# Optimization experiments

Hardware: AMD Instinct MI355X
Metric: run time of the kernel (lower is better)

## Reference

```python
import jax, jax.numpy as jnp
import numpy as np

N = 10000      # nodes
E = 80000      # directed edges (before self loops)
F_IN = 128     # input feature dim
OUT = 16       # out_channels (classes)


def setup_inputs() -> dict:
    key = jax.random.key(0)
    ks = jax.random.split(key, 20)
    p = lambda k, shape: (jax.random.normal(k, shape, jnp.float32) * 0.1)
    x = jax.random.normal(ks[0], (N, F_IN), jnp.float32)
    edge_index = jax.random.randint(ks[1], (2, E), 0, N, dtype=jnp.int64)
    return {
        "x": x, "edge_index": edge_index,
        # conv1: in=128 -> heads=10, ch=256
        "W1": p(ks[2], (F_IN, 10 * 256)), "as1": p(ks[3], (10, 256)), "ad1": p(ks[4], (10, 256)), "b1": jnp.zeros((10 * 256,), jnp.float32),
        # conv2: in=2560 -> heads=8, ch=56
        "W2": p(ks[5], (2560, 8 * 56)), "as2": p(ks[6], (8, 56)), "ad2": p(ks[7], (8, 56)), "b2": jnp.zeros((8 * 56,), jnp.float32),
        # conv3: in=448 -> heads=4, ch=32
        "W3": p(ks[8], (448, 4 * 32)), "as3": p(ks[9], (4, 32)), "ad3": p(ks[10], (4, 32)), "b3": jnp.zeros((4 * 32,), jnp.float32),
        # conv4: in=128 -> heads=1, ch=OUT, concat=False (mean over heads)
        "W4": p(ks[11], (128, 1 * OUT)), "as4": p(ks[12], (1, OUT)), "ad4": p(ks[13], (1, OUT)), "b4": jnp.zeros((OUT,), jnp.float32),
    }


def _gat_layer(x, src, dst, W, a_src, a_dst, b, heads, ch, concat, n):
    # linear projection -> [n, H, C]
    h = (x @ W).reshape(n, heads, ch)
    # per-node attention halves (PyG decomposition of a^T [h_i || h_j])
    e_src = jnp.einsum('nhc,hc->nh', h, a_src)
    e_dst = jnp.einsum('nhc,hc->nh', h, a_dst)
    # per-edge logits, LeakyReLU(0.2) as in PyG GATConv
    e = jax.nn.leaky_relu(e_src[src] + e_dst[dst], 0.2)  # [E', H]
    # segment softmax over edges grouped by destination node
    m = jax.ops.segment_max(e, dst, num_segments=n)
    m = jnp.where(jnp.isfinite(m), m, 0.0)
    ex = jnp.exp(e - m[dst])
    denom = jax.ops.segment_sum(ex, dst, num_segments=n)
    alpha = ex / (denom[dst] + 1e-16)  # [E', H]
    # weighted scatter-sum of source messages
    out = jax.ops.segment_sum(alpha[:, :, None] * h[src], dst, num_segments=n)  # [n, H, C]
    out = out.reshape(n, heads * ch) if concat else out.mean(axis=1)
    return out + b


def reference(x, edge_index, W1, as1, ad1, b1, W2, as2, ad2, b2,
              W3, as3, ad3, b3, W4, as4, ad4, b4):
    n = x.shape[0]
    loops = jnp.arange(n, dtype=edge_index.dtype)
    src = jnp.concatenate([edge_index[0], loops])  # add_self_loops=True
    dst = jnp.concatenate([edge_index[1], loops])
    lrelu = lambda t: jax.nn.leaky_relu(t, 0.1)  # outer activations in forward()
    h = lrelu(_gat_layer(x, src, dst, W1, as1, ad1, b1, 10, 256, True, n))
    h = lrelu(_gat_layer(h, src, dst, W2, as2, ad2, b2, 8, 56, True, n))
    h = lrelu(_gat_layer(h, src, dst, W3, as3, ad3, b3, 4, 32, True, n))
    h = lrelu(_gat_layer(h, src, dst, W4, as4, ad4, b4, 1, OUT, False, n))
    return jax.nn.softmax(h, axis=1)
```

## Files before the change

kernel.cpp:

```cpp
#include <hip/hip_runtime.h>
#include <math.h>

#define NNODES 10000
#define MPAD   10112
#define NEDGES 80000
#define ETOT   (NEDGES + NNODES)

typedef __attribute__((ext_vector_type(4))) float f32x4;
typedef __attribute__((ext_vector_type(8))) short bf16x8;
typedef __attribute__((ext_vector_type(4))) unsigned short u16x4;
typedef __attribute__((ext_vector_type(4))) unsigned int u32x4;

__device__ inline unsigned short f2bf(float f) {
    unsigned int u = __float_as_uint(f);
    unsigned int r = (u + 0x7fffu + ((u >> 16) & 1u)) >> 16;
    return (unsigned short)r;
}
__device__ inline float bf2f(unsigned short h) {
    return __uint_as_float(((unsigned int)h) << 16);
}
__device__ inline float lrelu01(float v) { return (v > 0.f) ? v : 0.1f * v; }
__device__ inline float lrelu02(float v) { return (v > 0.f) ? v : 0.2f * v; }

__global__ void count_deg(const int* __restrict__ ei, int* __restrict__ indeg,
                          int E, int n) {
    int i = blockIdx.x * blockDim.x + threadIdx.x;
    if (i >= E + n) return;
    int dst = (i < E) ? ei[E + i] : (i - E);
    atomicAdd(&indeg[dst], 1);
}

__global__ void scan_rowptr(const int* __restrict__ indeg, int* __restrict__ row_ptr,
                            int* __restrict__ cursor, int n) {
    __shared__ int sums[1024];
    int tid = threadIdx.x;
    int per = (n + 1023) / 1024;
    int start = tid * per;
    int end = start + per; if (end > n) end = n;
    int s = 0;
    for (int i = start; i < end; ++i) s += indeg[i];
    sums[tid] = s;
    __syncthreads();
    for (int off = 1; off < 1024; off <<= 1) {
        int v = (tid >= off) ? sums[tid - off] : 0;
        __syncthreads();
        sums[tid] += v;
        __syncthreads();
    }
    int excl = (tid == 0) ? 0 : sums[tid - 1];
    for (int i = start; i < end; ++i) {
        row_ptr[i] = excl;
        cursor[i]  = excl;
        excl += indeg[i];
    }
    if (tid == 1023) row_ptr[n] = sums[1023];
}

__global__ void scatter_edges(const int* __restrict__ ei, int* __restrict__ cursor,
                              int* __restrict__ col, int E, int n) {
    int i = blockIdx.x * blockDim.x + threadIdx.x;
    if (i >= E + n) return;
    int src, dst;
    if (i < E) { src = ei[i]; dst = ei[E + i]; }
    else       { src = i - E; dst = i - E; }
    int pos = atomicAdd(&cursor[dst], 1);
    col[pos] = src;
}

__global__ void convert_bf16(const float* __restrict__ in, unsigned short* __restrict__ out,
                             int n) {
    int i = blockIdx.x * blockDim.x + threadIdx.x;
    if (i < n) out[i] = f2bf(in[i]);
}

__global__ void transpose_all(const float* __restrict__ W1, const float* __restrict__ W2,
                              const float* __restrict__ W3,
                              unsigned short* __restrict__ W1t,
                              unsigned short* __restrict__ W2t,
                              unsigned short* __restrict__ W3t) {
    __shared__ float t[32][33];
    int b = blockIdx.x;
    const float* W; unsigned short* Wt; int K, N, nb, kb;
    if (b < 320)       { W = W1; Wt = W1t; K = 128;  N = 2560; int i = b;        nb = i % 80; kb = i / 80; }
    else if (b < 1440) { W = W2; Wt = W2t; K = 2560; N = 448;  int i = b - 320;  nb = i % 14; kb = i / 14; }
    else               { W = W3; Wt = W3t; K = 448;  N = 128;  int i = b - 1440; nb = i % 4;  kb = i / 4;  }
    int kb32 = kb * 32, nb32 = nb * 32;
    int tx = threadIdx.x, ty = threadIdx.y;
    #pragma unroll
    for (int i = 0; i < 32; i += 8)
        t[ty + i][tx] = W[(size_t)(kb32 + ty + i) * N + nb32 + tx];
    __syncthreads();
    #pragma unroll
    for (int i = 0; i < 32; i += 8)
        Wt[(size_t)(nb32 + ty + i) * K + kb32 + tx] = f2bf(t[tx][ty + i]);
}

#define GBM 128
#define GBK 32
template <int NT, bool SWIZ>
__global__ __launch_bounds__(256) void gemm_mfma(const unsigned short* __restrict__ A,
                                                 const unsigned short* __restrict__ Bt,
                                                 unsigned short* __restrict__ C,
                                                 int N, int nbn, int K, int klen) {
    constexpr int NI = NT / 32;
    __shared__ short As[GBM * GBK];
    __shared__ short Bs[NT * GBK];
    int bn, bm, kbeg, kend;
    size_t zoff = 0;
    if constexpr (SWIZ) {
        int b = blockIdx.x;
        int x = b & 7, t = b >> 3;
        int j = x + 8 * (t / nbn);
        if (j >= MPAD / GBM) return;
        bn = (t % nbn) * NT;
        bm = j * GBM;
        kbeg = blockIdx.y * klen;
        kend = kbeg + klen;
        zoff = (size_t)blockIdx.y * MPAD * N;
    } else {
        bn = blockIdx.x * NT;
        bm = blockIdx.y * GBM;
        kbeg = 0; kend = K;
    }
    int tid  = threadIdx.x;
    int wave = tid >> 6, lane = tid & 63;
    int wr = wave >> 1, wc = wave & 1;
    int lrow  = lane >> 2;
    int lkoff = (lane & 3) * 8;
    int row16 = lane & 15;
    int q8    = (lane >> 4) * 8;

    f32x4 acc[4][NI];
    #pragma unroll
    for (int mi = 0; mi < 4; ++mi)
        #pragma unroll
        for (int ni = 0; ni < NI; ++ni) acc[mi][ni] = (f32x4){0.f, 0.f, 0.f, 0.f};

    for (int k0 = kbeg; k0 < kend; k0 += GBK) {
        #pragma unroll
        for (int i = 0; i < 2; ++i) {
            int c = i * 4 + wave;
            int row = c * 16 + lrow;
            const unsigned short* gp = A + (size_t)(bm + row) * K + k0 + lkoff;
            __builtin_amdgcn_global_load_lds(
                (const __attribute__((address_space(1))) void*)gp,
                (__attribute__((address_space(3))) void*)&As[c * 512], 16, 0, 0);
        }
        #pragma unroll
        for (int i = 0; i < NT / 64; ++i) {
            int c = i * 4 + wave;
            int row = c * 16 + lrow;
            const unsigned short* gp = Bt + (size_t)(bn + row) * K + k0 + lkoff;
            __builtin_amdgcn_global_load_lds(
                (const __attribute__((address_space(1))) void*)gp,
                (__attribute__((address_space(3))) void*)&Bs[c * 512], 16, 0, 0);
        }
        __syncthreads();
        bf16x8 af[4], bfr[NI];
        #pragma unroll
        for (int mi = 0; mi < 4; ++mi)
            af[mi] = *(const bf16x8*)&As[(wr * 64 + mi * 16 + row16) * GBK + q8];
        #pragma unroll
        for (int ni = 0; ni < NI; ++ni)
            bfr[ni] = *(const bf16x8*)&Bs[(wc * (NT / 2) + ni * 16 + row16) * GBK + q8];
        #pragma unroll
        for (int mi = 0; mi < 4; ++mi)
            #pragma unroll
            for (int ni = 0; ni < NI; ++ni)
                acc[mi][ni] = __builtin_amdgcn_mfma_f32_16x16x32_bf16(
                    af[mi], bfr[ni], acc[mi][ni], 0, 0, 0);
        __syncthreads();
    }

    int rbase = bm + wr * 64 + (lane >> 4) * 4;
    int cbase = bn + wc * (NT / 2) + (lane & 15);
    #pragma unroll
    for (int mi = 0; mi < 4; ++mi)
        #pragma unroll
        for (int ni = 0; ni < NI; ++ni)
            #pragma unroll
            for (int r = 0; r < 4; ++r)
                C[zoff + (size_t)(rbase + mi * 16 + r) * N + cbase + ni * 16] =
                    f2bf(acc[mi][ni][r]);
}

__global__ void reduce2p(const unsigned int* __restrict__ P, unsigned int* __restrict__ out,
                         int n2) {
    int i = blockIdx.x * blockDim.x + threadIdx.x;
    if (i >= n2) return;
    unsigned int a = P[i];
    unsigned int b = P[(size_t)MPAD * 448 / 2 + i];
    float lo = bf2f((unsigned short)(a & 0xffffu)) + bf2f((unsigned short)(b & 0xffffu));
    float hi = bf2f((unsigned short)(a >> 16))     + bf2f((unsigned short)(b >> 16));
    out[i] = (unsigned int)f2bf(lo) | ((unsigned int)f2bf(hi) << 16);
}

__global__ __launch_bounds__(256) void gemm4_attn(const unsigned short* __restrict__ A,
                                                  const float* __restrict__ W,
                                                  const float* __restrict__ as4,
                                                  const float* __restrict__ ad4,
                                                  unsigned short* __restrict__ C,
                                                  float* __restrict__ e_src,
                                                  float* __restrict__ e_dst, int M) {
    __shared__ float Ws[128 * 16];
    int tid = threadIdx.x;
    for (int i = tid; i < 2048; i += 256) Ws[i] = W[i];
    __syncthreads();
    int node = blockIdx.x * 16 + (tid >> 4);
    int n = tid & 15;
    if (node >= M) return;
    const unsigned short* ap = A + (size_t)node * 128;
    float acc = 0.f;
    #pragma unroll 8
    for (int k = 0; k < 128; ++k)
        acc += bf2f(ap[k]) * Ws[k * 16 + n];
    C[(size_t)node * 16 + n] = f2bf(acc);
    float vs = acc * as4[n];
    float vd = acc * ad4[n];
    #pragma unroll
    for (int off = 1; off < 16; off <<= 1) {
        vs += __shfl_xor(vs, off);
        vd += __shfl_xor(vd, off);
    }
    if (n == 0) { e_src[node] = vs; e_dst[node] = vd; }
}

__global__ __launch_bounds__(64) void attn_halves(const unsigned short* __restrict__ h,
                                                  const float* __restrict__ a_src,
                                                  const float* __restrict__ a_dst,
                                                  float* __restrict__ e_src,
                                                  float* __restrict__ e_dst,
                                                  int H, int C) {
    int wid = blockIdx.x;
    int head = wid % H;
    int lane = threadIdx.x;
    const unsigned short* hp = h + (size_t)wid * C;
    float s1 = 0.f, s2 = 0.f;
    for (int c0 = lane * 4; c0 < C; c0 += 256) {
        u16x4 hv = *(const u16x4*)&hp[c0];
        f32x4 as = *(const f32x4*)&a_src[head * C + c0];
        f32x4 ad = *(const f32x4*)&a_dst[head * C + c0];
        #pragma unroll
        for (int j = 0; j < 4; ++j) {
            float v = bf2f(hv[j]);
            s1 += v * as[j];
            s2 += v * ad[j];
        }
    }
    #pragma unroll
    for (int off = 32; off; off >>= 1) {
        s1 += __shfl_down(s1, off);
        s2 += __shfl_down(s2, off);
    }
    if (lane == 0) { e_src[wid] = s1; e_dst[wid] = s2; }
}

template <int H, int C>
__global__ __launch_bounds__(64) void attn_small(const unsigned short* __restrict__ h,
                                                 const float* __restrict__ a_src,
                                                 const float* __restrict__ a_dst,
                                                 float* __restrict__ e_src,
                                                 float* __restrict__ e_dst) {
    constexpr int LPH = 64 / H;
    constexpr int CPL = C / LPH;
    int node = blockIdx.x;
    int lane = threadIdx.x;
    int head = lane / LPH;
    int k = lane - head * LPH;
    const unsigned short* hp = h + (size_t)node * (H * C) + head * C + k * CPL;
    const float* as = a_src + head * C + k * CPL;
    const float* ad = a_dst + head * C + k * CPL;
    float s1 = 0.f, s2 = 0.f;
    #pragma unroll
    for (int c = 0; c < CPL; ++c) {
        float v = bf2f(hp[c]);
        s1 += v * as[c];
        s2 += v * ad[c];
    }
    #pragma unroll
    for (int off = LPH / 2; off; off >>= 1) {
        s1 += __shfl_down(s1, off);
        s2 += __shfl_down(s2, off);
    }
    if (k == 0) { e_src[node * H + head] = s1; e_dst[node * H + head] = s2; }
}


__global__ __launch_bounds__(64) void agg_l1(const unsigned short* __restrict__ h,
                                             const float* __restrict__ e_src,
                                             const float* __restrict__ e_dst,
                                             const int* __restrict__ row_ptr,
                                             const int* __restrict__ col,
                                             const float* __restrict__ bias,
                                             unsigned short* __restrict__ out) {
    const int H = 10;
    int wid  = blockIdx.x;
    int node = wid / 5;
    int hp   = wid - node * 5;
    int lane = threadIdx.x;
    int sub  = lane >> 5;
    int head = hp * 2 + sub;
    int cpos = lane & 31;
    int rs = row_ptr[node], re = row_ptr[node + 1];
    float edv = e_dst[node * H + head];

    float dn = 0.f;
    float acc0[8], acc1[8];
    #pragma unroll
    for (int k = 0; k < 8; ++k) { acc0[k] = 0.f; acc1[k] = 0.f; }
    int i = rs;
    for (; i + 1 < re; i += 2) {
        int s0 = col[i], s1 = col[i + 1];
        float es0 = e_src[s0 * H + head];
        float es1 = e_src[s1 * H + head];
        u32x4 hv0 = *(const u32x4*)(h + (size_t)s0 * 2560 + head * 256 + cpos * 8);
        u32x4 hv1 = *(const u32x4*)(h + (size_t)s1 * 2560 + head * 256 + cpos * 8);
        float w0 = __expf(lrelu02(es0 + edv));
        float w1 = __expf(lrelu02(es1 + edv));
        dn += w0 + w1;
        #pragma unroll
        for (int d = 0; d < 4; ++d) {
            acc0[2 * d]     += w0 * bf2f((unsigned short)(hv0[d] & 0xffffu));
            acc0[2 * d + 1] += w0 * bf2f((unsigned short)(hv0[d] >> 16));
            acc1[2 * d]     += w1 * bf2f((unsigned short)(hv1[d] & 0xffffu));
            acc1[2 * d + 1] += w1 * bf2f((unsigned short)(hv1[d] >> 16));
        }
    }
    if (i < re) {
        int s = col[i];
        float w = __expf(lrelu02(e_src[s * H + head] + edv));
        dn += w;
        u32x4 hv = *(const u32x4*)(h + (size_t)s * 2560 + head * 256 + cpos * 8);
        #pragma unroll
        for (int d = 0; d < 4; ++d) {
            acc0[2 * d]     += w * bf2f((unsigned short)(hv[d] & 0xffffu));
            acc0[2 * d + 1] += w * bf2f((unsigned short)(hv[d] >> 16));
        }
    }
    float rdn = 1.f / (dn + 1e-16f);

    const float* bp = bias + head * 256 + cpos * 8;
    u32x4 o;
    #pragma unroll
    for (int d = 0; d < 4; ++d) {
        float v0 = lrelu01((acc0[2 * d] + acc1[2 * d]) * rdn + bp[2 * d]);
        float v1 = lrelu01((acc0[2 * d + 1] + acc1[2 * d + 1]) * rdn + bp[2 * d + 1]);
        o[d] = (unsigned int)f2bf(v0) | ((unsigned int)f2bf(v1) << 16);
    }
    *(u32x4*)(out + (size_t)node * 2560 + head * 256 + cpos * 8) = o;
}

__global__ __launch_bounds__(64) void agg_l2(const unsigned short* __restrict__ h,
                                             const float* __restrict__ e_src,
                                             const float* __restrict__ e_dst,
                                             const int* __restrict__ row_ptr,
                                             const int* __restrict__ col,
                                             const float* __restrict__ bias,
                                             unsigned short* __restrict__ out) {
    const int H = 8;
    int node = blockIdx.x;
    int lane = threadIdx.x;
    bool act = lane < 56;
    int head = act ? (lane / 7) : 0;
    int cpos = act ? (lane - head * 7) : 0;
    int rs = row_ptr[node], re = row_ptr[node + 1];
    float edv = e_dst[node * H + head];

    float dn = 0.f;
    float acc0[8], acc1[8];
    #pragma unroll
    for (int k = 0; k < 8; ++k) { acc0[k] = 0.f; acc1[k] = 0.f; }
    int i = rs;
    for (; i + 1 < re; i += 2) {
        int s0 = col[i], s1 = col[i + 1];
        float es0 = e_src[s0 * H + head];
        float es1 = e_src[s1 * H + head];
        u32x4 hv0 = *(const u32x4*)(h + (size_t)s0 * 448 + head * 56 + cpos * 8);
        u32x4 hv1 = *(const u32x4*)(h + (size_t)s1 * 448 + head * 56 + cpos * 8);
        float w0 = __expf(lrelu02(es0 + edv));
        float w1 = __expf(lrelu02(es1 + edv));
        dn += w0 + w1;
        #pragma unroll
        for (int d = 0; d < 4; ++d) {
            acc0[2 * d]     += w0 * bf2f((unsigned short)(hv0[d] & 0xffffu));
            acc0[2 * d + 1] += w0 * bf2f((unsigned short)(hv0[d] >> 16));
            acc1[2 * d]     += w1 * bf2f((unsigned short)(hv1[d] & 0xffffu));
            acc1[2 * d + 1] += w1 * bf2f((unsigned short)(hv1[d] >> 16));
        }
    }
    if (i < re) {
        int s = col[i];
        float w = __expf(lrelu02(e_src[s * H + head] + edv));
        dn += w;
        u32x4 hv = *(const u32x4*)(h + (size_t)s * 448 + head * 56 + cpos * 8);
        #pragma unroll
        for (int d = 0; d < 4; ++d) {
            acc0[2 * d]     += w * bf2f((unsigned short)(hv[d] & 0xffffu));
            acc0[2 * d + 1] += w * bf2f((unsigned short)(hv[d] >> 16));
        }
    }
    float rdn = 1.f / (dn + 1e-16f);

    if (act) {
        const float* bp = bias + head * 56 + cpos * 8;
        u32x4 o;
        #pragma unroll
        for (int d = 0; d < 4; ++d) {
            float v0 = lrelu01((acc0[2 * d] + acc1[2 * d]) * rdn + bp[2 * d]);
            float v1 = lrelu01((acc0[2 * d + 1] + acc1[2 * d + 1]) * rdn + bp[2 * d + 1]);
            o[d] = (unsigned int)f2bf(v0) | ((unsigned int)f2bf(v1) << 16);
        }
        *(u32x4*)(out + (size_t)node * 448 + head * 56 + cpos * 8) = o;
    }
}

__global__ __launch_bounds__(64) void agg_l3(const unsigned short* __restrict__ h,
                                             const float* __restrict__ e_src,
                                             const float* __restrict__ e_dst,
                                             const int* __restrict__ row_ptr,
                                             const int* __restrict__ col,
                                             const float* __restrict__ bias,
                                             unsigned short* __restrict__ out) {
    const int H = 4;
    int node = blockIdx.x;
    int lane = threadIdx.x;
    bool act = lane < 16;
    int head = (lane >> 2) & 3;
    int cpos = lane & 3;
    int rs = row_ptr[node], re = row_ptr[node + 1];
    float edv = e_dst[node * H + head];

    float dn = 0.f;
    float acc0[8], acc1[8];
    #pragma unroll
    for (int k = 0; k < 8; ++k) { acc0[k] = 0.f; acc1[k] = 0.f; }
    int i = rs;
    for (; i + 1 < re; i += 2) {
        int s0 = col[i], s1 = col[i + 1];
        float es0 = e_src[s0 * H + head];
        float es1 = e_src[s1 * H + head];
        u32x4 hv0 = *(const u32x4*)(h + (size_t)s0 * 128 + head * 32 + cpos * 8);
        u32x4 hv1 = *(const u32x4*)(h + (size_t)s1 * 128 + head * 32 + cpos * 8);
        float w0 = __expf(lrelu02(es0 + edv));
        float w1 = __expf(lrelu02(es1 + edv));
        dn += w0 + w1;
        #pragma unroll
        for (int d = 0; d < 4; ++d) {
            acc0[2 * d]     += w0 * bf2f((unsigned short)(hv0[d] & 0xffffu));
            acc0[2 * d + 1] += w0 * bf2f((unsigned short)(hv0[d] >> 16));
            acc1[2 * d]     += w1 * bf2f((unsigned short)(hv1[d] & 0xffffu));
            acc1[2 * d + 1] += w1 * bf2f((unsigned short)(hv1[d] >> 16));
        }
    }
    if (i < re) {
        int s = col[i];
        float w = __expf(lrelu02(e_src[s * H + head] + edv));
        dn += w;
        u32x4 hv = *(const u32x4*)(h + (size_t)s * 128 + head * 32 + cpos * 8);
        #pragma unroll
        for (int d = 0; d < 4; ++d) {
            acc0[2 * d]     += w * bf2f((unsigned short)(hv[d] & 0xffffu));
            acc0[2 * d + 1] += w * bf2f((unsigned short)(hv[d] >> 16));
        }
    }
    float rdn = 1.f / (dn + 1e-16f);

    if (act) {
        const float* bp = bias + head * 32 + cpos * 8;
        u32x4 o;
        #pragma unroll
        for (int d = 0; d < 4; ++d) {
            float v0 = lrelu01((acc0[2 * d] + acc1[2 * d]) * rdn + bp[2 * d]);
            float v1 = lrelu01((acc0[2 * d + 1] + acc1[2 * d + 1]) * rdn + bp[2 * d + 1]);
            o[d] = (unsigned int)f2bf(v0) | ((unsigned int)f2bf(v1) << 16);
        }
        *(u32x4*)(out + (size_t)node * 128 + head * 32 + cpos * 8) = o;
    }
}

__global__ __launch_bounds__(64) void agg4_softmax(const unsigned int* __restrict__ h2,
                                                   const float* __restrict__ e_src,
                                                   const float* __restrict__ e_dst,
                                                   const int* __restrict__ row_ptr,
                                                   const int* __restrict__ col,
                                                   const float* __restrict__ bias,
                                                   float* __restrict__ out) {
    int node = blockIdx.x;
    int lane = threadIdx.x;
    int cpos = lane & 7;
    int rs = row_ptr[node], re = row_ptr[node + 1];
    float edv = e_dst[node];

    float dn = 0.f, a0 = 0.f, a1 = 0.f;
    for (int i = rs; i < re; ++i) {
        int s = col[i];
        float w = __expf(lrelu02(e_src[s] + edv));
        dn += w;
        unsigned int hv = h2[(size_t)s * 8 + cpos];
        a0 += w * bf2f((unsigned short)(hv & 0xffffu));
        a1 += w * bf2f((unsigned short)(hv >> 16));
    }
    float rdn = 1.f / (dn + 1e-16f);
    float v0 = lrelu01(a0 * rdn + bias[2 * cpos]);
    float v1 = lrelu01(a1 * rdn + bias[2 * cpos + 1]);

    float m = fmaxf(v0, v1);
    #pragma unroll
    for (int off = 4; off; off >>= 1) m = fmaxf(m, __shfl_xor(m, off));
    float e0 = __expf(v0 - m), e1 = __expf(v1 - m);
    float s = e0 + e1;
    #pragma unroll
    for (int off = 4; off; off >>= 1) s += __shfl_xor(s, off);
    float r = 1.f / s;
    if (lane < 8) {
        out[node * 16 + 2 * cpos]     = e0 * r;
        out[node * 16 + 2 * cpos + 1] = e1 * r;
    }
}

extern "C" void kernel_launch(void* const* d_in, const int* in_sizes, int n_in,
                              void* d_out, int out_size, void* d_ws, size_t ws_size,
                              hipStream_t stream) {
    const float* x   = (const float*)d_in[0];
    const int*   ei  = (const int*)d_in[1];
    const float* W1  = (const float*)d_in[2];
    const float* as1 = (const float*)d_in[3];
    const float* ad1 = (const float*)d_in[4];
    const float* b1  = (const float*)d_in[5];
    const float* W2  = (const float*)d_in[6];
    const float* as2 = (const float*)d_in[7];
    const float* ad2 = (const float*)d_in[8];
    const float* b2  = (const float*)d_in[9];
    const float* W3  = (const float*)d_in[10];
    const float* as3 = (const float*)d_in[11];
    const float* ad3 = (const float*)d_in[12];
    const float* b3  = (const float*)d_in[13];
    const float* W4  = (const float*)d_in[14];
    const float* as4 = (const float*)d_in[15];
    const float* ad4 = (const float*)d_in[16];
    const float* b4  = (const float*)d_in[17];

    char* ws = (char*)d_ws;
    size_t off = 0;
    auto alloc = [&](size_t bytes) -> void* {
        void* p = ws + off;
        off = (off + bytes + 255) & ~(size_t)255;
        return p;
    };
    unsigned short* hbuf = (unsigned short*)alloc((size_t)MPAD * 2560 * sizeof(short));
    unsigned short* abuf = (unsigned short*)alloc((size_t)MPAD * 2560 * sizeof(short));
    unsigned short* pbuf = (unsigned short*)alloc((size_t)2 * MPAD * 448 * sizeof(short));
    unsigned short* W1t  = (unsigned short*)alloc((size_t)2560 * 128 * sizeof(short));
    unsigned short* W2t  = (unsigned short*)alloc((size_t)448 * 2560 * sizeof(short));
    unsigned short* W3t  = (unsigned short*)alloc((size_t)128 * 448 * sizeof(short));
    float* e_src  = (float*)alloc((size_t)NNODES * 10 * sizeof(float));
    float* e_dst  = (float*)alloc((size_t)NNODES * 10 * sizeof(float));
    int* indeg    = (int*)alloc(NNODES * sizeof(int));
    int* row_ptr  = (int*)alloc((NNODES + 1) * sizeof(int));
    int* cursor   = (int*)alloc(NNODES * sizeof(int));
    int* col      = (int*)alloc(ETOT * sizeof(int));
    (void)ws_size;

    hipMemsetAsync(indeg, 0, NNODES * sizeof(int), stream);
    int eb = (ETOT + 255) / 256;
    count_deg<<<eb, 256, 0, stream>>>(ei, indeg, NEDGES, NNODES);
    scan_rowptr<<<1, 1024, 0, stream>>>(indeg, row_ptr, cursor, NNODES);
    scatter_edges<<<eb, 256, 0, stream>>>(ei, cursor, col, NEDGES, NNODES);

    transpose_all<<<1496, dim3(32, 8), 0, stream>>>(W1, W2, W3, W1t, W2t, W3t);
    convert_bf16<<<(NNODES * 128 + 255) / 256, 256, 0, stream>>>(x, abuf, NNODES * 128);

    const int Mb = MPAD / GBM;

    gemm_mfma<128, false><<<dim3(2560 / 128, Mb), 256, 0, stream>>>(
        abuf, W1t, hbuf, 2560, 1, 128, 128);
    attn_halves<<<NNODES * 10, 64, 0, stream>>>(hbuf, as1, ad1, e_src, e_dst, 10, 256);
    agg_l1<<<NNODES * 5, 64, 0, stream>>>(hbuf, e_src, e_dst, row_ptr, col, b1, abuf);

    gemm_mfma<64, true><<<dim3(8 * 7 * 10, 2), 256, 0, stream>>>(
        abuf, W2t, pbuf, 448, 7, 2560, 1280);
    {
        int n2 = NNODES * 448 / 2;
        reduce2p<<<(n2 + 255) / 256, 256, 0, stream>>>(
            (const unsigned int*)pbuf, (unsigned int*)hbuf, n2);
    }
    attn_small<8, 56><<<NNODES, 64, 0, stream>>>(hbuf, as2, ad2, e_src, e_dst);
    agg_l2<<<NNODES, 64, 0, stream>>>(hbuf, e_src, e_dst, row_ptr, col, b2, abuf);

    gemm_mfma<64, false><<<dim3(2, Mb), 256, 0, stream>>>(
        abuf, W3t, hbuf, 128, 1, 448, 448);
    attn_small<4, 32><<<NNODES, 64, 0, stream>>>(hbuf, as3, ad3, e_src, e_dst);
    agg_l3<<<NNODES, 64, 0, stream>>>(hbuf, e_src, e_dst, row_ptr, col, b3, abuf);

    gemm4_attn<<<(NNODES + 15) / 16, 256, 0, stream>>>(
        abuf, W4, as4, ad4, hbuf, e_src, e_dst, NNODES);
    agg4_softmax<<<NNODES, 64, 0, stream>>>(
        (const unsigned int*)hbuf, e_src, e_dst, row_ptr, col, b4, (float*)d_out);
}
```

Measured before the change: 347.6 us.

## Reorder layer-1 GAT as aggregate-then-project with precomputed attention weight vectors

```diff
diff --git a/kernel.cpp b/kernel.cpp
--- a/kernel.cpp
+++ b/kernel.cpp
@@ -8,7 +8,6 @@
 
 typedef __attribute__((ext_vector_type(4))) float f32x4;
 typedef __attribute__((ext_vector_type(8))) short bf16x8;
-typedef __attribute__((ext_vector_type(4))) unsigned short u16x4;
 typedef __attribute__((ext_vector_type(4))) unsigned int u32x4;
 
 __device__ inline unsigned short f2bf(float f) {
@@ -95,8 +94,172 @@
         Wt[(size_t)(nb32 + ty + i) * K + kb32 + tx] = f2bf(t[tx][ty + i]);
 }
 
+__global__ void make_wsd(const float* __restrict__ W1, const float* __restrict__ as1,
+                         const float* __restrict__ ad1,
+                         float* __restrict__ wsrc, float* __restrict__ wdst) {
+    int idx = blockIdx.x * blockDim.x + threadIdx.x;
+    if (idx >= 1280) return;
+    int h = idx >> 7, k = idx & 127;
+    const float* wrow = W1 + (size_t)k * 2560 + h * 256;
+    const float* as = as1 + h * 256;
+    const float* ad = ad1 + h * 256;
+    float s = 0.f, d = 0.f;
+    for (int c = 0; c < 256; c += 4) {
+        f32x4 w = *(const f32x4*)&wrow[c];
+        f32x4 a = *(const f32x4*)&as[c];
+        f32x4 b = *(const f32x4*)&ad[c];
+        #pragma unroll
+        for (int j = 0; j < 4; ++j) { s += w[j] * a[j]; d += w[j] * b[j]; }
+    }
+    wsrc[h * 128 + k] = s;
+    wdst[h * 128 + k] = d;
+}
+
+__global__ __launch_bounds__(256) void e1_dots(const unsigned short* __restrict__ xb,
+                                               const float* __restrict__ wsrc,
+                                               const float* __restrict__ wdst,
+                                               float* __restrict__ e_src,
+                                               float* __restrict__ e_dst, int M) {
+    __shared__ float ws[1280], wd[1280];
+    int tid = threadIdx.x;
+    for (int i = tid; i < 1280; i += 256) { ws[i] = wsrc[i]; wd[i] = wdst[i]; }
+    __syncthreads();
+    int node = blockIdx.x * 4 + (tid >> 6);
+    int lane = tid & 63;
+    if (node >= M) return;
+    unsigned int xv = ((const unsigned int*)xb)[node * 64 + lane];
+    float v0 = bf2f((unsigned short)(xv & 0xffffu));
+    float v1 = bf2f((unsigned short)(xv >> 16));
+    #pragma unroll
+    for (int h = 0; h < 10; ++h) {
+        float ps = v0 * ws[h * 128 + 2 * lane] + v1 * ws[h * 128 + 2 * lane + 1];
+        float pd = v0 * wd[h * 128 + 2 * lane] + v1 * wd[h * 128 + 2 * lane + 1];
+        #pragma unroll
+        for (int off = 32; off; off >>= 1) {
+            ps += __shfl_down(ps, off);
+            pd += __shfl_down(pd, off);
+        }
+        if (lane == 0) { e_src[node * 10 + h] = ps; e_dst[node * 10 + h] = pd; }
+    }
+}
+
+__global__ __launch_bounds__(64) void agg_x(const unsigned short* __restrict__ xb,
+                                            const float* __restrict__ e_src,
+                                            const float* __restrict__ e_dst,
+                                            const int* __restrict__ row_ptr,
+                                            const int* __restrict__ col,
+                                            unsigned short* __restrict__ xagg) {
+    int node = blockIdx.x;
+    int lane = threadIdx.x;
+    int rs = row_ptr[node], re = row_ptr[node + 1];
+    float edv = (lane < 10) ? e_dst[node * 10 + lane] : 0.f;
+
+    float dn = 0.f;
+    float a0[10], a1[10];
+    #pragma unroll
+    for (int h = 0; h < 10; ++h) { a0[h] = 0.f; a1[h] = 0.f; }
+    for (int i = rs; i < re; ++i) {
+        int s = col[i];
+        float w = 0.f;
+        if (lane < 10) w = __expf(lrelu02(e_src[s * 10 + lane] + edv));
+        dn += w;
+        unsigned int xv = ((const unsigned int*)xb)[s * 64 + lane];
+        float v0 = bf2f((unsigned short)(xv & 0xffffu));
+        float v1 = bf2f((unsigned short)(xv >> 16));
+        #pragma unroll
+        for (int h = 0; h < 10; ++h) {
+            float wh = __shfl(w, h);
+            a0[h] += wh * v0;
+            a1[h] += wh * v1;
+        }
+    }
+    #pragma unroll
+    for (int h = 0; h < 10; ++h) {
+        float rdn = 1.f / (__shfl(dn, h) + 1e-16f);
+        unsigned int o = (unsigned int)f2bf(a0[h] * rdn) |
+                         ((unsigned int)f2bf(a1[h] * rdn) << 16);
+        ((unsigned int*)xagg)[((size_t)node * 10 + h) * 64 + lane] = o;
+    }
+}
+
 #define GBM 128
 #define GBK 32
+__global__ __launch_bounds__(256) void gemm_l1(const unsigned short* __restrict__ A,
+                                               const unsigned short* __restrict__ Bt,
+                                               const float* __restrict__ bias,
+                                               unsigned short* __restrict__ C) {
+    constexpr int NT = 128, NI = 4, K = 128;
+    __shared__ short As[GBM * GBK];
+    __shared__ short Bs[NT * GBK];
+    int h  = blockIdx.x >> 1;
+    int nt = blockIdx.x & 1;
+    int bn = h * 256 + nt * 128;
+    int bm = blockIdx.y * GBM;
+    int tid  = threadIdx.x;
+    int wave = tid >> 6, lane = tid & 63;
+    int wr = wave >> 1, wc = wave & 1;
+    int lrow  = lane >> 2;
+    int lkoff = (lane & 3) * 8;
+    int row16 = lane & 15;
+    int q8    = (lane >> 4) * 8;
+
+    f32x4 acc[4][NI];
+    #pragma unroll
+    for (int mi = 0; mi < 4; ++mi)
+        #pragma unroll
+        for (int ni = 0; ni < NI; ++ni) acc[mi][ni] = (f32x4){0.f, 0.f, 0.f, 0.f};
+
+    for (int k0 = 0; k0 < K; k0 += GBK) {
+        #pragma unroll
+        for (int i = 0; i < 2; ++i) {
+            int c = i * 4 + wave;
+            int row = c * 16 + lrow;
+            const unsigned short* gp = A + ((size_t)(bm + row) * 10 + h) * K + k0 + lkoff;
+            __builtin_amdgcn_global_load_lds(
+                (const __attribute__((address_space(1))) void*)gp,
+                (__attribute__((address_space(3))) void*)&As[c * 512], 16, 0, 0);
+        }
+        #pragma unroll
+        for (int i = 0; i < 2; ++i) {
+            int c = i * 4 + wave;
+            int row = c * 16 + lrow;
+            const unsigned short* gp = Bt + (size_t)(bn + row) * K + k0 + lkoff;
+            __builtin_amdgcn_global_load_lds(
+                (const __attribute__((address_space(1))) void*)gp,
+                (__attribute__((address_space(3))) void*)&Bs[c * 512], 16, 0, 0);
+        }
+        __syncthreads();
+        bf16x8 af[4], bfr[NI];
+        #pragma unroll
+        for (int mi = 0; mi < 4; ++mi)
+            af[mi] = *(const bf16x8*)&As[(wr * 64 + mi * 16 + row16) * GBK + q8];
+        #pragma unroll
+        for (int ni = 0; ni < NI; ++ni)
+            bfr[ni] = *(const bf16x8*)&Bs[(wc * 64 + ni * 16 + row16) * GBK + q8];
+        #pragma unroll
+        for (int mi = 0; mi < 4; ++mi)
+            #pragma unroll
+            for (int ni = 0; ni < NI; ++ni)
+                acc[mi][ni] = __builtin_amdgcn_mfma_f32_16x16x32_bf16(
+                    af[mi], bfr[ni], acc[mi][ni], 0, 0, 0);
+        __syncthreads();
+    }
+
+    int rbase = bm + wr * 64 + (lane >> 4) * 4;
+    #pragma unroll
+    for (int mi = 0; mi < 4; ++mi)
+        #pragma unroll
+        for (int ni = 0; ni < NI; ++ni) {
+            int cc = bn + wc * 64 + ni * 16 + (lane & 15);
+            float b = bias[cc];
+            #pragma unroll
+            for (int r = 0; r < 4; ++r) {
+                float v = lrelu01(acc[mi][ni][r] + b);
+                C[(size_t)(rbase + mi * 16 + r) * 2560 + cc] = f2bf(v);
+            }
+        }
+}
+
 template <int NT, bool SWIZ>
 __global__ __launch_bounds__(256) void gemm_mfma(const unsigned short* __restrict__ A,
                                                  const unsigned short* __restrict__ Bt,
@@ -225,36 +388,6 @@
     if (n == 0) { e_src[node] = vs; e_dst[node] = vd; }
 }
 
-__global__ __launch_bounds__(64) void attn_halves(const unsigned short* __restrict__ h,
-                                                  const float* __restrict__ a_src,
-                                                  const float* __restrict__ a_dst,
-                                                  float* __restrict__ e_src,
-                                                  float* __restrict__ e_dst,
-                                                  int H, int C) {
-    int wid = blockIdx.x;
-    int head = wid % H;
-    int lane = threadIdx.x;
-    const unsigned short* hp = h + (size_t)wid * C;
-    float s1 = 0.f, s2 = 0.f;
-    for (int c0 = lane * 4; c0 < C; c0 += 256) {
-        u16x4 hv = *(const u16x4*)&hp[c0];
-        f32x4 as = *(const f32x4*)&a_src[head * C + c0];
-        f32x4 ad = *(const f32x4*)&a_dst[head * C + c0];
-        #pragma unroll
-        for (int j = 0; j < 4; ++j) {
-            float v = bf2f(hv[j]);
-            s1 += v * as[j];
-            s2 += v * ad[j];
-        }
-    }
-    #pragma unroll
-    for (int off = 32; off; off >>= 1) {
-        s1 += __shfl_down(s1, off);
-        s2 += __shfl_down(s2, off);
-    }
-    if (lane == 0) { e_src[wid] = s1; e_dst[wid] = s2; }
-}
-
 template <int H, int C>
 __global__ __launch_bounds__(64) void attn_small(const unsigned short* __restrict__ h,
                                                  const float* __restrict__ a_src,
@@ -283,71 +416,6 @@
         s2 += __shfl_down(s2, off);
     }
     if (k == 0) { e_src[node * H + head] = s1; e_dst[node * H + head] = s2; }
-}
-
-
-__global__ __launch_bounds__(64) void agg_l1(const unsigned short* __restrict__ h,
-                                             const float* __restrict__ e_src,
-                                             const float* __restrict__ e_dst,
-                                             const int* __restrict__ row_ptr,
-                                             const int* __restrict__ col,
-                                             const float* __restrict__ bias,
-                                             unsigned short* __restrict__ out) {
-    const int H = 10;
-    int wid  = blockIdx.x;
-    int node = wid / 5;
-    int hp   = wid - node * 5;
-    int lane = threadIdx.x;
-    int sub  = lane >> 5;
-    int head = hp * 2 + sub;
-    int cpos = lane & 31;
-    int rs = row_ptr[node], re = row_ptr[node + 1];
-    float edv = e_dst[node * H + head];
-
-    float dn = 0.f;
-    float acc0[8], acc1[8];
-    #pragma unroll
-    for (int k = 0; k < 8; ++k) { acc0[k] = 0.f; acc1[k] = 0.f; }
-    int i = rs;
-    for (; i + 1 < re; i += 2) {
-        int s0 = col[i], s1 = col[i + 1];
-        float es0 = e_src[s0 * H + head];
-        float es1 = e_src[s1 * H + head];
-        u32x4 hv0 = *(const u32x4*)(h + (size_t)s0 * 2560 + head * 256 + cpos * 8);
-        u32x4 hv1 = *(const u32x4*)(h + (size_t)s1 * 2560 + head * 256 + cpos * 8);
-        float w0 = __expf(lrelu02(es0 + edv));
-        float w1 = __expf(lrelu02(es1 + edv));
-        dn += w0 + w1;
-        #pragma unroll
-        for (int d = 0; d < 4; ++d) {
-            acc0[2 * d]     += w0 * bf2f((unsigned short)(hv0[d] & 0xffffu));
-            acc0[2 * d + 1] += w0 * bf2f((unsigned short)(hv0[d] >> 16));
-            acc1[2 * d]     += w1 * bf2f((unsigned short)(hv1[d] & 0xffffu));
-            acc1[2 * d + 1] += w1 * bf2f((unsigned short)(hv1[d] >> 16));
-        }
-    }
-    if (i < re) {
-        int s = col[i];
-        float w = __expf(lrelu02(e_src[s * H + head] + edv));
-        dn += w;
-        u32x4 hv = *(const u32x4*)(h + (size_t)s * 2560 + head * 256 + cpos * 8);
-        #pragma unroll
-        for (int d = 0; d < 4; ++d) {
-            acc0[2 * d]     += w * bf2f((unsigned short)(hv[d] & 0xffffu));
-            acc0[2 * d + 1] += w * bf2f((unsigned short)(hv[d] >> 16));
-        }
-    }
-    float rdn = 1.f / (dn + 1e-16f);
-
-    const float* bp = bias + head * 256 + cpos * 8;
-    u32x4 o;
-    #pragma unroll
-    for (int d = 0; d < 4; ++d) {
-        float v0 = lrelu01((acc0[2 * d] + acc1[2 * d]) * rdn + bp[2 * d]);
-        float v1 = lrelu01((acc0[2 * d + 1] + acc1[2 * d + 1]) * rdn + bp[2 * d + 1]);
-        o[d] = (unsigned int)f2bf(v0) | ((unsigned int)f2bf(v1) << 16);
-    }
-    *(u32x4*)(out + (size_t)node * 2560 + head * 256 + cpos * 8) = o;
 }
 
 __global__ __launch_bounds__(64) void agg_l2(const unsigned short* __restrict__ h,
@@ -550,9 +618,12 @@
     unsigned short* hbuf = (unsigned short*)alloc((size_t)MPAD * 2560 * sizeof(short));
     unsigned short* abuf = (unsigned short*)alloc((size_t)MPAD * 2560 * sizeof(short));
     unsigned short* pbuf = (unsigned short*)alloc((size_t)2 * MPAD * 448 * sizeof(short));
+    unsigned short* xagg = (unsigned short*)alloc((size_t)MPAD * 10 * 128 * sizeof(short));
     unsigned short* W1t  = (unsigned short*)alloc((size_t)2560 * 128 * sizeof(short));
     unsigned short* W2t  = (unsigned short*)alloc((size_t)448 * 2560 * sizeof(short));
     unsigned short* W3t  = (unsigned short*)alloc((size_t)128 * 448 * sizeof(short));
+    float* wsrc   = (float*)alloc((size_t)10 * 128 * sizeof(float));
+    float* wdst   = (float*)alloc((size_t)10 * 128 * sizeof(float));
     float* e_src  = (float*)alloc((size_t)NNODES * 10 * sizeof(float));
     float* e_dst  = (float*)alloc((size_t)NNODES * 10 * sizeof(float));
     int* indeg    = (int*)alloc(NNODES * sizeof(int));
@@ -568,14 +639,14 @@
     scatter_edges<<<eb, 256, 0, stream>>>(ei, cursor, col, NEDGES, NNODES);
 
     transpose_all<<<1496, dim3(32, 8), 0, stream>>>(W1, W2, W3, W1t, W2t, W3t);
+    make_wsd<<<20, 64, 0, stream>>>(W1, as1, ad1, wsrc, wdst);
     convert_bf16<<<(NNODES * 128 + 255) / 256, 256, 0, stream>>>(x, abuf, NNODES * 128);
 
     const int Mb = MPAD / GBM;
 
-    gemm_mfma<128, false><<<dim3(2560 / 128, Mb), 256, 0, stream>>>(
-        abuf, W1t, hbuf, 2560, 1, 128, 128);
-    attn_halves<<<NNODES * 10, 64, 0, stream>>>(hbuf, as1, ad1, e_src, e_dst, 10, 256);
-    agg_l1<<<NNODES * 5, 64, 0, stream>>>(hbuf, e_src, e_dst, row_ptr, col, b1, abuf);
+    e1_dots<<<(NNODES + 3) / 4, 256, 0, stream>>>(abuf, wsrc, wdst, e_src, e_dst, NNODES);
+    agg_x<<<NNODES, 64, 0, stream>>>(abuf, e_src, e_dst, row_ptr, col, xagg);
+    gemm_l1<<<dim3(20, Mb), 256, 0, stream>>>(xagg, W1t, b1, abuf);
 
     gemm_mfma<64, true><<<dim3(8 * 7 * 10, 2), 256, 0, stream>>>(
         abuf, W2t, pbuf, 448, 7, 2560, 1280);
```

Result: faster. 301.4 us (-13.3%).
